# Kernel optimization log

Measured on AMD Instinct MI355X. Metric: run time of the kernel, lower is better.

The kernel has to match this reference:

```python
import jax, jax.numpy as jnp
import numpy as np

C = 256          # channels
NH = 8           # heads
DH = 64          # dim_head
NMEM = 4         # num_mem_kv
HIDDEN = NH * DH # 512
SCALE = DH ** (-0.5)


def _rmsnorm(x, gain):
    # F.normalize(x, dim=1) * gain * sqrt(C)  (scale-only RMS norm over channel dim)
    n = jnp.sqrt(jnp.sum(x * x, axis=1, keepdims=True))
    return x / jnp.maximum(n, 1e-12) * gain * (x.shape[1] ** 0.5)


def setup_inputs() -> dict:
    key = jax.random.key(0)
    ks = jax.random.split(key, 6)
    B, Hh, Ww = 16, 64, 64
    return {
        "x": jax.random.normal(ks[0], (B, C, Hh, Ww), jnp.float32),
        "gain1": jnp.ones((1, C, 1, 1), jnp.float32),
        "w_qkv": jax.random.normal(ks[1], (3 * HIDDEN, C), jnp.float32) * 0.02,
        "mem_kv": jax.random.normal(ks[2], (2, NH, DH, NMEM), jnp.float32),
        "w_out": jax.random.normal(ks[3], (C, HIDDEN), jnp.float32) * 0.02,
        "b_out": jnp.zeros((C,), jnp.float32),
        "gain2": jnp.ones((1, C, 1, 1), jnp.float32),
    }


def reference(x, gain1, w_qkv, mem_kv, w_out, b_out, gain2):
    B, _, Hh, Ww = x.shape
    N = Hh * Ww
    # pre-norm
    xn = _rmsnorm(x, gain1)
    # 1x1 conv QKV projection (no bias) == channel GEMM
    qkv = jnp.einsum('oc,bchw->bohw', w_qkv, xn)          # [B, 3*hidden, H, W]
    qkv = qkv.reshape(B, 3, NH, DH, N)                    # chunk + 'b (h c) x y -> b h c (x y)'
    q, k, v = qkv[:, 0], qkv[:, 1], qkv[:, 2]             # [B, h, d, N]
    # learned global memory kv, broadcast over batch
    mem_k = jnp.broadcast_to(mem_kv[0], (B, NH, DH, NMEM))
    mem_v = jnp.broadcast_to(mem_kv[1], (B, NH, DH, NMEM))
    k = jnp.concatenate([mem_k, k], axis=-1)              # [B, h, d, NMEM+N]
    v = jnp.concatenate([mem_v, v], axis=-1)
    # dual softmax: q over feature dim d, k over token dim n
    q = jax.nn.softmax(q, axis=-2) * SCALE
    k = jax.nn.softmax(k, axis=-1)
    # linear attention: O(N) context
    context = jnp.einsum('bhdn,bhen->bhde', k, v)         # [B, h, d, e]
    out = jnp.einsum('bhde,bhdn->bhen', context, q)       # [B, h, e, N]
    out = out.reshape(B, HIDDEN, Hh, Ww)
    # 1x1 conv out projection (with bias) + post RMSNorm
    out = jnp.einsum('oc,bchw->bohw', w_out, out) + b_out[None, :, None, None]
    return _rmsnorm(out, gain2)
```

## Files before the change

### kernel.cpp

```cpp
#include <hip/hip_runtime.h>

typedef __attribute__((ext_vector_type(8))) short bf16x8;
typedef __attribute__((ext_vector_type(4))) short bf16x4;
typedef __attribute__((ext_vector_type(4))) float f32x4;
typedef unsigned short u16;

constexpr int B_   = 16;
constexpr int C_   = 256;
constexpr int NH   = 8;
constexpr int DH   = 64;
constexpr int NMEM = 4;
constexpr int HID  = 512;
constexpr int QKVC = 1536;
constexpr int N_   = 4096;
constexpr int CTXS = 4224;

__device__ __forceinline__ u16 f2b(float f) {
  union { float f; unsigned u; } v{f};
  unsigned r = v.u + 0x7fff + ((v.u >> 16) & 1);
  return (u16)(r >> 16);
}
__device__ __forceinline__ float b2f(u16 h) {
  union { unsigned u; float f; } v; v.u = ((unsigned)h) << 16; return v.f;
}

__device__ __forceinline__ void gld_lds16(const u16* g, u16* l) {
  __builtin_amdgcn_global_load_lds(
      (const __attribute__((address_space(1))) unsigned*)g,
      (__attribute__((address_space(3))) unsigned*)l, 16, 0, 0);
}

__global__ void k_cvtw(const float* __restrict__ wq, const float* __restrict__ wo,
                       u16* __restrict__ wqb, u16* __restrict__ wob) {
  int i = blockIdx.x * 256 + threadIdx.x;
  for (int idx = i; idx < QKVC * C_; idx += gridDim.x * 256) wqb[idx] = f2b(wq[idx]);
  for (int idx = i; idx < C_ * HID; idx += gridDim.x * 256) wob[idx] = f2b(wo[idx]);
}

__global__ __launch_bounds__(256) void k_rms1(const float* __restrict__ x,
                                              const float* __restrict__ g1,
                                              u16* __restrict__ xbT) {
  int g = blockIdx.y;
  int n = blockIdx.x * 256 + threadIdx.x;
  const float* xp = x + (size_t)g * C_ * N_ + n;
  float ss = 0.f;
  #pragma unroll 8
  for (int c = 0; c < C_; ++c) { float v = xp[(size_t)c * N_]; ss += v * v; }
  float inv = 16.0f / fmaxf(sqrtf(ss), 1e-12f);
  u16* op = xbT + ((size_t)g * N_ + n) * C_;
  for (int c0 = 0; c0 < C_; c0 += 8) {
    union { bf16x8 v; u16 u[8]; } pk;
    #pragma unroll
    for (int j = 0; j < 8; ++j) pk.u[j] = f2b(xp[(size_t)(c0 + j) * N_] * inv * g1[c0 + j]);
    *(bf16x8*)(op + c0) = pk.v;
  }
}

__global__ __launch_bounds__(256) void k_kvctx(const u16* __restrict__ Wb,
                                               const u16* __restrict__ XT,
                                               float* __restrict__ ctxp) {
  constexpr int BK = 32;
  __shared__ __align__(16) u16 smem[16384];
  u16* Ws = smem;
  u16* Xs = smem + 4096;
  u16* Pl = smem;
  u16* Vl = smem + 8192;

  int cpx = gridDim.x >> 3;
  int bid = blockIdx.x;
  int L = (bid & 7) * cpx + (bid >> 3);
  int h = L & 7, nc = (L >> 3) & 7, g = L >> 6;
  int t = threadIdx.x, wave = t >> 6, lane = t & 63;
  int wm = wave >> 1, wn = wave & 1;
  int kg = lane >> 4, lr = lane & 15;

  const u16* WK = Wb + (size_t)(HID + h * DH) * C_;
  const u16* WV = Wb + (size_t)(2 * HID + h * DH) * C_;
  const u16* Xg = XT + ((size_t)g * N_ + nc * 512) * C_;

  int rloc = lane >> 2;
  int cswz = (lane & 3) ^ (rloc & 3);
  const u16* Wsrc = (wave < 2) ? WK : WV;
  int wrow0 = (wave * 32) & 63;

  f32x4 acc2[4];
  #pragma unroll
  for (int nf = 0; nf < 4; ++nf) acc2[nf] = (f32x4)0.f;
  float rs[4] = {0.f, 0.f, 0.f, 0.f};

  for (int it = 0; it < 4; ++it) {
    f32x4 acc[4][4];
    #pragma unroll
    for (int i = 0; i < 4; ++i)
      #pragma unroll
      for (int j = 0; j < 4; ++j) acc[i][j] = (f32x4)0.f;

    for (int k0 = 0; k0 < C_; k0 += BK) {
      #pragma unroll
      for (int q = 0; q < 2; ++q) {
        int rw = wrow0 + q * 16 + rloc;
        int rx = wave * 32 + q * 16 + rloc;
        gld_lds16(Wsrc + (size_t)rw * C_ + k0 + cswz * 8, Ws + (wave * 32 + q * 16) * 32);
        gld_lds16(Xg + (size_t)(it * 128 + rx) * C_ + k0 + cswz * 8, Xs + (wave * 32 + q * 16) * 32);
      }
      __syncthreads();
      bf16x8 a[4], bv[4];
      #pragma unroll
      for (int mf = 0; mf < 4; ++mf) {
        int r = wm * 64 + mf * 16 + lr;
        a[mf] = *(const bf16x8*)(Xs + r * 32 + ((kg ^ (r & 3)) * 8));
      }
      #pragma unroll
      for (int nf = 0; nf < 4; ++nf) {
        int r = wn * 64 + nf * 16 + lr;
        bv[nf] = *(const bf16x8*)(Ws + r * 32 + ((kg ^ (r & 3)) * 8));
      }
      #pragma unroll
      for (int mf = 0; mf < 4; ++mf)
        #pragma unroll
        for (int nf = 0; nf < 4; ++nf)
          acc[mf][nf] = __builtin_amdgcn_mfma_f32_16x16x32_bf16(a[mf], bv[nf], acc[mf][nf], 0, 0, 0);
      __syncthreads();
    }

    if (wn == 0) {
      #pragma unroll
      for (int mf = 0; mf < 4; ++mf) {
        int nb = wm * 64 + mf * 16 + kg * 4;
        int cc = nb >> 3, off = nb & 7;
        #pragma unroll
        for (int nf = 0; nf < 4; ++nf) {
          int d = nf * 16 + lr;
          float e0 = __expf(acc[mf][nf][0]);
          float e1 = __expf(acc[mf][nf][1]);
          float e2 = __expf(acc[mf][nf][2]);
          float e3 = __expf(acc[mf][nf][3]);
          rs[nf] += (e0 + e1) + (e2 + e3);
          union { bf16x4 v; u16 u[4]; } pk;
          pk.u[0] = f2b(e0); pk.u[1] = f2b(e1); pk.u[2] = f2b(e2); pk.u[3] = f2b(e3);
          *(bf16x4*)(Pl + d * 128 + ((cc ^ (d & 15)) * 8) + off) = pk.v;
        }
      }
    } else {
      #pragma unroll
      for (int mf = 0; mf < 4; ++mf) {
        int nb = wm * 64 + mf * 16 + kg * 4;
        int cc = nb >> 3, off = nb & 7;
        #pragma unroll
        for (int nf = 0; nf < 4; ++nf) {
          int e = nf * 16 + lr;
          union { bf16x4 v; u16 u[4]; } pk;
          pk.u[0] = f2b(acc[mf][nf][0]); pk.u[1] = f2b(acc[mf][nf][1]);
          pk.u[2] = f2b(acc[mf][nf][2]); pk.u[3] = f2b(acc[mf][nf][3]);
          *(bf16x4*)(Vl + e * 128 + ((cc ^ (e & 15)) * 8) + off) = pk.v;
        }
      }
    }
    __syncthreads();

    #pragma unroll
    for (int k = 0; k < 4; ++k) {
      int c = k * 4 + kg;
      bf16x8 af = *(const bf16x8*)(Pl + (wave * 16 + lr) * 128 + ((c ^ lr) * 8));
      #pragma unroll
      for (int nf = 0; nf < 4; ++nf) {
        bf16x8 bfv = *(const bf16x8*)(Vl + (nf * 16 + lr) * 128 + ((c ^ lr) * 8));
        acc2[nf] = __builtin_amdgcn_mfma_f32_16x16x32_bf16(af, bfv, acc2[nf], 0, 0, 0);
      }
    }
    __syncthreads();
  }

  float* cgp = ctxp + ((size_t)(g * NH + h) * 8 + nc) * CTXS;
  #pragma unroll
  for (int nf = 0; nf < 4; ++nf)
    #pragma unroll
    for (int j = 0; j < 4; ++j) {
      int d = wave * 16 + kg * 4 + j;
      int e = nf * 16 + lr;
      cgp[d * 64 + e] = acc2[nf][j];
    }
  if (wn == 0) {
    #pragma unroll
    for (int nf = 0; nf < 4; ++nf) {
      rs[nf] += __shfl_xor(rs[nf], 16);
      rs[nf] += __shfl_xor(rs[nf], 32);
    }
    if (lane < 16) {
      #pragma unroll
      for (int nf = 0; nf < 4; ++nf)
        cgp[4096 + wm * 64 + nf * 16 + lane] = rs[nf];
    }
  }
}

__global__ __launch_bounds__(256) void k_cfin(const float* __restrict__ ctxp,
                                              const float* __restrict__ memkv,
                                              u16* __restrict__ ctxTb) {
  int g = blockIdx.y, h = blockIdx.x;
  int t = threadIdx.x;
  __shared__ float emk[DH * NMEM];
  __shared__ float sd[DH];
  const float* mk = memkv + (size_t)h * DH * NMEM;
  const float* mv = memkv + (size_t)(NH + h) * DH * NMEM;
  const float* cp = ctxp + (size_t)(g * NH + h) * 8 * CTXS;
  emk[t] = __expf(mk[t]);
  __syncthreads();
  if (t < DH) {
    float s = 0.f;
    #pragma unroll
    for (int p = 0; p < 8; ++p)
      s += cp[p * CTXS + 4096 + t] + cp[p * CTXS + 4160 + t];
    #pragma unroll
    for (int j = 0; j < NMEM; ++j) s += emk[t * 4 + j];
    sd[t] = s;
  }
  __syncthreads();
  u16* ct = ctxTb + (size_t)(g * NH + h) * 4096;
  #pragma unroll
  for (int i = 0; i < 16; ++i) {
    int idx = t + 256 * i;
    int d = idx >> 6, e = idx & 63;
    float v = 0.f;
    #pragma unroll
    for (int p = 0; p < 8; ++p) v += cp[p * CTXS + idx];
    #pragma unroll
    for (int j = 0; j < NMEM; ++j) v += emk[d * 4 + j] * mv[e * 4 + j];
    ct[e * 64 + d] = f2b(v / sd[d]);
  }
}

__global__ __launch_bounds__(256) void k_qpv(const u16* __restrict__ Wq,
                                             const u16* __restrict__ XT,
                                             const u16* __restrict__ ctxTb,
                                             u16* __restrict__ attnT) {
  constexpr int BK = 32;
  __shared__ __align__(16) u16 smem[24576];
  u16* Ws = smem;
  u16* Xs = smem + 4096;
  u16* cl = smem + 16384;

  int cpx = gridDim.x >> 3;
  int bid = blockIdx.x;
  int L = (bid & 7) * cpx + (bid >> 3);
  int hh = L & 3, rest = L >> 2;
  int nc = rest & 31, g = rest >> 5;
  int t = threadIdx.x, wave = t >> 6, lane = t & 63;
  int wm = wave >> 1, wn = wave & 1;
  int kg = lane >> 4, lr = lane & 15;

  {
    const u16* cg = ctxTb + (size_t)(g * NH + hh * 2) * 4096;
    #pragma unroll
    for (int i = 0; i < 4; ++i) {
      int id = t + 256 * i;
      int r = id >> 3, c = id & 7;
      *(bf16x8*)(cl + (r >> 6) * 4096 + (r & 63) * 64 + ((c ^ (r & 7)) * 8)) =
          *(const bf16x8*)(cg + id * 8);
    }
  }

  const u16* Ag = Wq + (size_t)(hh * 128) * C_;
  const u16* Bg = XT + ((size_t)g * N_ + nc * 128) * C_;
  int rloc = lane >> 2;
  int cswz = (lane & 3) ^ (rloc & 3);

  f32x4 acc[4][4];
  #pragma unroll
  for (int i = 0; i < 4; ++i)
    #pragma unroll
    for (int j = 0; j < 4; ++j) acc[i][j] = (f32x4)0.f;

  for (int k0 = 0; k0 < C_; k0 += BK) {
    #pragma unroll
    for (int q = 0; q < 2; ++q) {
      int r = wave * 32 + q * 16 + rloc;
      gld_lds16(Ag + (size_t)r * C_ + k0 + cswz * 8, Ws + (wave * 32 + q * 16) * 32);
      gld_lds16(Bg + (size_t)r * C_ + k0 + cswz * 8, Xs + (wave * 32 + q * 16) * 32);
    }
    __syncthreads();
    bf16x8 a[4], bv[4];
    #pragma unroll
    for (int mf = 0; mf < 4; ++mf) {
      int r = wm * 64 + mf * 16 + lr;
      a[mf] = *(const bf16x8*)(Ws + r * 32 + ((kg ^ (r & 3)) * 8));
    }
    #pragma unroll
    for (int nf = 0; nf < 4; ++nf) {
      int r = wn * 64 + nf * 16 + lr;
      bv[nf] = *(const bf16x8*)(Xs + r * 32 + ((kg ^ (r & 3)) * 8));
    }
    #pragma unroll
    for (int mf = 0; mf < 4; ++mf)
      #pragma unroll
      for (int nf = 0; nf < 4; ++nf)
        acc[mf][nf] = __builtin_amdgcn_mfma_f32_16x16x32_bf16(a[mf], bv[nf], acc[mf][nf], 0, 0, 0);
    __syncthreads();
  }

  float colsum[4];
  #pragma unroll
  for (int nf = 0; nf < 4; ++nf) {
    float s = 0.f;
    #pragma unroll
    for (int mf = 0; mf < 4; ++mf)
      #pragma unroll
      for (int j = 0; j < 4; ++j) {
        float e = __expf(acc[mf][nf][j]);
        acc[mf][nf][j] = e;
        s += e;
      }
    colsum[nf] = s;
  }
  #pragma unroll
  for (int nf = 0; nf < 4; ++nf) {
    colsum[nf] += __shfl_xor(colsum[nf], 16);
    colsum[nf] += __shfl_xor(colsum[nf], 32);
  }
  u16* qh = smem + wm * 8192;
  #pragma unroll
  for (int nf = 0; nf < 4; ++nf) {
    float invs = 0.125f / colsum[nf];
    int n = wn * 64 + nf * 16 + lr;
    #pragma unroll
    for (int mf = 0; mf < 4; ++mf)
      #pragma unroll
      for (int jp = 0; jp < 2; ++jp) {
        int d0 = mf * 16 + kg * 4 + jp * 2;
        u16 lo = f2b(acc[mf][nf][jp * 2] * invs);
        u16 hi = f2b(acc[mf][nf][jp * 2 + 1] * invs);
        unsigned pk = (unsigned)lo | ((unsigned)hi << 16);
        int idx = n * 64 + (((d0 >> 3) ^ (n & 7)) * 8) + (d0 & 7);
        *(unsigned*)(qh + idx) = pk;
      }
  }
  __syncthreads();

  int hcl = wave >> 1, nh2 = wave & 1;
  const u16* qh2 = smem + hcl * 8192;
  const u16* clh = cl + hcl * 4096;
  f32x4 acc2[4][4];
  #pragma unroll
  for (int i = 0; i < 4; ++i)
    #pragma unroll
    for (int j = 0; j < 4; ++j) acc2[i][j] = (f32x4)0.f;

  #pragma unroll
  for (int kk = 0; kk < 2; ++kk) {
    int c = kk * 4 + kg;
    bf16x8 a2[4], b2[4];
    #pragma unroll
    for (int mf = 0; mf < 4; ++mf) {
      int rn = nh2 * 64 + mf * 16 + lr;
      a2[mf] = *(const bf16x8*)(qh2 + rn * 64 + ((c ^ (rn & 7)) * 8));
    }
    #pragma unroll
    for (int nf = 0; nf < 4; ++nf) {
      int re = nf * 16 + lr;
      b2[nf] = *(const bf16x8*)(clh + re * 64 + ((c ^ (re & 7)) * 8));
    }
    #pragma unroll
    for (int mf = 0; mf < 4; ++mf)
      #pragma unroll
      for (int nf = 0; nf < 4; ++nf)
        acc2[mf][nf] = __builtin_amdgcn_mfma_f32_16x16x32_bf16(a2[mf], b2[nf], acc2[mf][nf], 0, 0, 0);
  }

  int h = hh * 2 + hcl;
  u16* op = attnT + ((size_t)g * N_ + nc * 128) * HID + h * 64;
  #pragma unroll
  for (int mf = 0; mf < 4; ++mf)
    #pragma unroll
    for (int nf = 0; nf < 4; ++nf)
      #pragma unroll
      for (int j = 0; j < 4; ++j) {
        int n = nh2 * 64 + mf * 16 + kg * 4 + j;
        int e = nf * 16 + lr;
        op[(size_t)n * HID + e] = f2b(acc2[mf][nf][j]);
      }
}

__global__ __launch_bounds__(256) void k_out(const u16* __restrict__ Wb,
                                             const u16* __restrict__ AT,
                                             const float* __restrict__ bias,
                                             const float* __restrict__ g2,
                                             float* __restrict__ out) {
  constexpr int BN = 128, BK = 32;
  __shared__ __align__(16) u16 As[256 * BK];
  __shared__ __align__(16) u16 Bs[BN * BK];
  __shared__ float part[4][BN];
  int g  = blockIdx.y;
  int n0 = blockIdx.x * BN;
  int t = threadIdx.x, wave = t >> 6, lane = t & 63;
  int kg = lane >> 4, lr = lane & 15;

  const u16* Bg = AT + ((size_t)g * N_ + n0) * HID;

  int rloc = lane >> 2;
  int cswz = (lane & 3) ^ (rloc & 3);

  f32x4 acc[4][8];
  #pragma unroll
  for (int i = 0; i < 4; ++i)
    #pragma unroll
    for (int j = 0; j < 8; ++j) acc[i][j] = (f32x4)0.f;

  for (int k0 = 0; k0 < HID; k0 += BK) {
    #pragma unroll
    for (int q = 0; q < 4; ++q) {
      int r = wave * 64 + q * 16 + rloc;
      gld_lds16(Wb + (size_t)r * HID + k0 + cswz * 8, As + (wave * 64 + q * 16) * 32);
    }
    #pragma unroll
    for (int q = 0; q < 2; ++q) {
      int r = wave * 32 + q * 16 + rloc;
      gld_lds16(Bg + (size_t)r * HID + k0 + cswz * 8, Bs + (wave * 32 + q * 16) * 32);
    }
    __syncthreads();
    bf16x8 a[4], bv[8];
    #pragma unroll
    for (int mf = 0; mf < 4; ++mf) {
      int r = wave * 64 + mf * 16 + lr;
      a[mf] = *(const bf16x8*)(As + r * 32 + ((kg ^ (r & 3)) * 8));
    }
    #pragma unroll
    for (int nf = 0; nf < 8; ++nf) {
      int r = nf * 16 + lr;
      bv[nf] = *(const bf16x8*)(Bs + r * 32 + ((kg ^ (r & 3)) * 8));
    }
    #pragma unroll
    for (int mf = 0; mf < 4; ++mf)
      #pragma unroll
      for (int nf = 0; nf < 8; ++nf)
        acc[mf][nf] = __builtin_amdgcn_mfma_f32_16x16x32_bf16(a[mf], bv[nf], acc[mf][nf], 0, 0, 0);
    __syncthreads();
  }
  float colsq[8] = {0.f, 0.f, 0.f, 0.f, 0.f, 0.f, 0.f, 0.f};
  #pragma unroll
  for (int mf = 0; mf < 4; ++mf)
    #pragma unroll
    for (int j = 0; j < 4; ++j) {
      int row = wave * 64 + mf * 16 + kg * 4 + j;
      float bs = bias[row];
      #pragma unroll
      for (int nf = 0; nf < 8; ++nf) {
        float v = acc[mf][nf][j] + bs;
        acc[mf][nf][j] = v;
        colsq[nf] += v * v;
      }
    }
  #pragma unroll
  for (int nf = 0; nf < 8; ++nf) {
    colsq[nf] += __shfl_xor(colsq[nf], 16);
    colsq[nf] += __shfl_xor(colsq[nf], 32);
  }
  if (kg == 0) {
    #pragma unroll
    for (int nf = 0; nf < 8; ++nf) part[wave][nf * 16 + lr] = colsq[nf];
  }
  __syncthreads();
  float* og = out + (size_t)g * C_ * N_ + n0;
  #pragma unroll
  for (int nf = 0; nf < 8; ++nf) {
    int col = nf * 16 + lr;
    float tot = part[0][col] + part[1][col] + part[2][col] + part[3][col];
    float invn = 16.0f / fmaxf(sqrtf(tot), 1e-12f);
    #pragma unroll
    for (int mf = 0; mf < 4; ++mf)
      #pragma unroll
      for (int j = 0; j < 4; ++j) {
        int row = wave * 64 + mf * 16 + kg * 4 + j;
        og[(size_t)row * N_ + col] = acc[mf][nf][j] * invn * g2[row];
      }
  }
}

extern "C" void kernel_launch(void* const* d_in, const int* in_sizes, int n_in,
                              void* d_out, int out_size, void* d_ws, size_t ws_size,
                              hipStream_t stream) {
  (void)in_sizes; (void)n_in; (void)out_size;
  const float* x      = (const float*)d_in[0];
  const float* gain1  = (const float*)d_in[1];
  const float* w_qkv  = (const float*)d_in[2];
  const float* mem_kv = (const float*)d_in[3];
  const float* w_out  = (const float*)d_in[4];
  const float* b_out  = (const float*)d_in[5];
  const float* gain2  = (const float*)d_in[6];
  float* out = (float*)d_out;

  char* ws = (char*)d_ws;
  u16* wqkvb = (u16*)ws;
  u16* woutb = (u16*)(ws + 786432);
  size_t shared_b = 1048576;

  const size_t xbT_b   = (size_t)N_ * C_ * 2;
  const size_t attnT_b = (size_t)HID * N_ * 2;
  const size_t ctxp_b  = (size_t)NH * 8 * CTXS * 4;
  const size_t ctxT_b  = (size_t)NH * 4096 * 2;
  const size_t per_b   = xbT_b + attnT_b + ctxp_b + ctxT_b;

  int G = 16;
  while (G > 1 && shared_b + (size_t)G * per_b > ws_size) G >>= 1;

  char* base = ws + shared_b;
  u16*   xbT   = (u16*)base;
  u16*   attnT = (u16*)(base + (size_t)G * xbT_b);
  float* ctxp  = (float*)(base + (size_t)G * (xbT_b + attnT_b));
  u16*   ctxTb = (u16*)(base + (size_t)G * (xbT_b + attnT_b + ctxp_b));

  k_cvtw<<<256, 256, 0, stream>>>(w_qkv, w_out, wqkvb, woutb);

  for (int b0 = 0; b0 < B_; b0 += G) {
    const float* xc = x + (size_t)b0 * C_ * N_;
    float*       oc = out + (size_t)b0 * C_ * N_;
    k_rms1  <<<dim3(N_ / 256, G),  256, 0, stream>>>(xc, gain1, xbT);
    k_kvctx <<<dim3(64 * G),       256, 0, stream>>>(wqkvb, xbT, ctxp);
    k_cfin  <<<dim3(NH, G),        256, 0, stream>>>(ctxp, mem_kv, ctxTb);
    k_qpv   <<<dim3(4 * 32 * G),   256, 0, stream>>>(wqkvb, xbT, ctxTb, attnT);
    k_out   <<<dim3(N_ / 128, G),  256, 0, stream>>>(woutb, attnT, b_out, gain2, oc);
  }
}
```

Before: 199.4 us.

## Double GEMM K-tile to 64 with 8-way swizzle and vectorize RMS norm loads

The three MFMA GEMM kernels (kvctx, qpv, out) now stage a 64-wide K tile per iteration instead of 32, using an 8-chunk XOR swizzle. This halves the number of barrier pairs per K loop and does two MFMA k-steps per staged tile, at the cost of more LDS per block. Separately, the pre-norm kernel has each thread handle 4 adjacent pixels with float4 loads and launches a quarter as many blocks. That widens global reads but leaves fewer threads in flight for a bandwidth-bound pass.

New measurement: 205.0 us. 2.8% more time.

```diff
diff --git a/kernel.cpp b/kernel.cpp
--- a/kernel.cpp
+++ b/kernel.cpp
@@ -41,28 +41,41 @@
                                               const float* __restrict__ g1,
                                               u16* __restrict__ xbT) {
   int g = blockIdx.y;
-  int n = blockIdx.x * 256 + threadIdx.x;
-  const float* xp = x + (size_t)g * C_ * N_ + n;
-  float ss = 0.f;
-  #pragma unroll 8
-  for (int c = 0; c < C_; ++c) { float v = xp[(size_t)c * N_]; ss += v * v; }
-  float inv = 16.0f / fmaxf(sqrtf(ss), 1e-12f);
-  u16* op = xbT + ((size_t)g * N_ + n) * C_;
+  int n0 = (blockIdx.x * 256 + threadIdx.x) * 4;
+  const float* xg = x + (size_t)g * C_ * N_;
+  float ss0 = 0.f, ss1 = 0.f, ss2 = 0.f, ss3 = 0.f;
+  #pragma unroll 4
+  for (int c = 0; c < C_; ++c) {
+    float4 v = *(const float4*)(xg + (size_t)c * N_ + n0);
+    ss0 += v.x * v.x; ss1 += v.y * v.y; ss2 += v.z * v.z; ss3 += v.w * v.w;
+  }
+  float inv0 = 16.0f / fmaxf(sqrtf(ss0), 1e-12f);
+  float inv1 = 16.0f / fmaxf(sqrtf(ss1), 1e-12f);
+  float inv2 = 16.0f / fmaxf(sqrtf(ss2), 1e-12f);
+  float inv3 = 16.0f / fmaxf(sqrtf(ss3), 1e-12f);
+  u16* op = xbT + ((size_t)g * N_ + n0) * C_;
   for (int c0 = 0; c0 < C_; c0 += 8) {
-    union { bf16x8 v; u16 u[8]; } pk;
-    #pragma unroll
-    for (int j = 0; j < 8; ++j) pk.u[j] = f2b(xp[(size_t)(c0 + j) * N_] * inv * g1[c0 + j]);
-    *(bf16x8*)(op + c0) = pk.v;
+    union { bf16x8 v; u16 u[8]; } p0, p1, p2, p3;
+    #pragma unroll
+    for (int j = 0; j < 8; ++j) {
+      float4 v = *(const float4*)(xg + (size_t)(c0 + j) * N_ + n0);
+      float gc = g1[c0 + j];
+      p0.u[j] = f2b(v.x * inv0 * gc); p1.u[j] = f2b(v.y * inv1 * gc);
+      p2.u[j] = f2b(v.z * inv2 * gc); p3.u[j] = f2b(v.w * inv3 * gc);
+    }
+    *(bf16x8*)(op + c0)          = p0.v;
+    *(bf16x8*)(op + C_ + c0)     = p1.v;
+    *(bf16x8*)(op + 2 * C_ + c0) = p2.v;
+    *(bf16x8*)(op + 3 * C_ + c0) = p3.v;
   }
 }
 
 __global__ __launch_bounds__(256) void k_kvctx(const u16* __restrict__ Wb,
                                                const u16* __restrict__ XT,
                                                float* __restrict__ ctxp) {
-  constexpr int BK = 32;
   __shared__ __align__(16) u16 smem[16384];
   u16* Ws = smem;
-  u16* Xs = smem + 4096;
+  u16* Xs = smem + 8192;
   u16* Pl = smem;
   u16* Vl = smem + 8192;
 
@@ -78,10 +91,9 @@
   const u16* WV = Wb + (size_t)(2 * HID + h * DH) * C_;
   const u16* Xg = XT + ((size_t)g * N_ + nc * 512) * C_;
 
-  int rloc = lane >> 2;
-  int cswz = (lane & 3) ^ (rloc & 3);
+  int rl8 = lane >> 3;
+  int cs8 = (lane & 7) ^ rl8;
   const u16* Wsrc = (wave < 2) ? WK : WV;
-  int wrow0 = (wave * 32) & 63;
 
   f32x4 acc2[4];
   #pragma unroll
@@ -95,31 +107,36 @@
       #pragma unroll
       for (int j = 0; j < 4; ++j) acc[i][j] = (f32x4)0.f;
 
-    for (int k0 = 0; k0 < C_; k0 += BK) {
-      #pragma unroll
-      for (int q = 0; q < 2; ++q) {
-        int rw = wrow0 + q * 16 + rloc;
-        int rx = wave * 32 + q * 16 + rloc;
-        gld_lds16(Wsrc + (size_t)rw * C_ + k0 + cswz * 8, Ws + (wave * 32 + q * 16) * 32);
-        gld_lds16(Xg + (size_t)(it * 128 + rx) * C_ + k0 + cswz * 8, Xs + (wave * 32 + q * 16) * 32);
+    for (int k0 = 0; k0 < C_; k0 += 64) {
+      #pragma unroll
+      for (int q = 0; q < 4; ++q) {
+        int rb = wave * 32 + q * 8;
+        int rw = (rb & 63) + rl8;
+        int rx = it * 128 + rb + rl8;
+        gld_lds16(Wsrc + (size_t)rw * C_ + k0 + cs8 * 8, Ws + rb * 64);
+        gld_lds16(Xg + (size_t)rx * C_ + k0 + cs8 * 8, Xs + rb * 64);
       }
       __syncthreads();
-      bf16x8 a[4], bv[4];
-      #pragma unroll
-      for (int mf = 0; mf < 4; ++mf) {
-        int r = wm * 64 + mf * 16 + lr;
-        a[mf] = *(const bf16x8*)(Xs + r * 32 + ((kg ^ (r & 3)) * 8));
-      }
-      #pragma unroll
-      for (int nf = 0; nf < 4; ++nf) {
-        int r = wn * 64 + nf * 16 + lr;
-        bv[nf] = *(const bf16x8*)(Ws + r * 32 + ((kg ^ (r & 3)) * 8));
-      }
-      #pragma unroll
-      for (int mf = 0; mf < 4; ++mf)
-        #pragma unroll
-        for (int nf = 0; nf < 4; ++nf)
-          acc[mf][nf] = __builtin_amdgcn_mfma_f32_16x16x32_bf16(a[mf], bv[nf], acc[mf][nf], 0, 0, 0);
+      #pragma unroll
+      for (int ks = 0; ks < 2; ++ks) {
+        int ch = ks * 4 + kg;
+        bf16x8 a[4], bv[4];
+        #pragma unroll
+        for (int mf = 0; mf < 4; ++mf) {
+          int r = wm * 64 + mf * 16 + lr;
+          a[mf] = *(const bf16x8*)(Xs + r * 64 + ((ch ^ (r & 7)) * 8));
+        }
+        #pragma unroll
+        for (int nf = 0; nf < 4; ++nf) {
+          int r = wn * 64 + nf * 16 + lr;
+          bv[nf] = *(const bf16x8*)(Ws + r * 64 + ((ch ^ (r & 7)) * 8));
+        }
+        #pragma unroll
+        for (int mf = 0; mf < 4; ++mf)
+          #pragma unroll
+          for (int nf = 0; nf < 4; ++nf)
+            acc[mf][nf] = __builtin_amdgcn_mfma_f32_16x16x32_bf16(a[mf], bv[nf], acc[mf][nf], 0, 0, 0);
+      }
       __syncthreads();
     }
 
@@ -234,10 +251,9 @@
                                              const u16* __restrict__ XT,
                                              const u16* __restrict__ ctxTb,
                                              u16* __restrict__ attnT) {
-  constexpr int BK = 32;
   __shared__ __align__(16) u16 smem[24576];
   u16* Ws = smem;
-  u16* Xs = smem + 4096;
+  u16* Xs = smem + 8192;
   u16* cl = smem + 16384;
 
   int cpx = gridDim.x >> 3;
@@ -262,8 +278,8 @@
 
   const u16* Ag = Wq + (size_t)(hh * 128) * C_;
   const u16* Bg = XT + ((size_t)g * N_ + nc * 128) * C_;
-  int rloc = lane >> 2;
-  int cswz = (lane & 3) ^ (rloc & 3);
+  int rl8 = lane >> 3;
+  int cs8 = (lane & 7) ^ rl8;
 
   f32x4 acc[4][4];
   #pragma unroll
@@ -271,30 +287,34 @@
     #pragma unroll
     for (int j = 0; j < 4; ++j) acc[i][j] = (f32x4)0.f;
 
-  for (int k0 = 0; k0 < C_; k0 += BK) {
-    #pragma unroll
-    for (int q = 0; q < 2; ++q) {
-      int r = wave * 32 + q * 16 + rloc;
-      gld_lds16(Ag + (size_t)r * C_ + k0 + cswz * 8, Ws + (wave * 32 + q * 16) * 32);
-      gld_lds16(Bg + (size_t)r * C_ + k0 + cswz * 8, Xs + (wave * 32 + q * 16) * 32);
+  for (int k0 = 0; k0 < C_; k0 += 64) {
+    #pragma unroll
+    for (int q = 0; q < 4; ++q) {
+      int rb = wave * 32 + q * 8;
+      gld_lds16(Ag + (size_t)(rb + rl8) * C_ + k0 + cs8 * 8, Ws + rb * 64);
+      gld_lds16(Bg + (size_t)(rb + rl8) * C_ + k0 + cs8 * 8, Xs + rb * 64);
     }
     __syncthreads();
-    bf16x8 a[4], bv[4];
-    #pragma unroll
-    for (int mf = 0; mf < 4; ++mf) {
-      int r = wm * 64 + mf * 16 + lr;
-      a[mf] = *(const bf16x8*)(Ws + r * 32 + ((kg ^ (r & 3)) * 8));
-    }
-    #pragma unroll
-    for (int nf = 0; nf < 4; ++nf) {
-      int r = wn * 64 + nf * 16 + lr;
-      bv[nf] = *(const bf16x8*)(Xs + r * 32 + ((kg ^ (r & 3)) * 8));
-    }
-    #pragma unroll
-    for (int mf = 0; mf < 4; ++mf)
-      #pragma unroll
-      for (int nf = 0; nf < 4; ++nf)
-        acc[mf][nf] = __builtin_amdgcn_mfma_f32_16x16x32_bf16(a[mf], bv[nf], acc[mf][nf], 0, 0, 0);
+    #pragma unroll
+    for (int ks = 0; ks < 2; ++ks) {
+      int ch = ks * 4 + kg;
+      bf16x8 a[4], bv[4];
+      #pragma unroll
+      for (int mf = 0; mf < 4; ++mf) {
+        int r = wm * 64 + mf * 16 + lr;
+        a[mf] = *(const bf16x8*)(Ws + r * 64 + ((ch ^ (r & 7)) * 8));
+      }
+      #pragma unroll
+      for (int nf = 0; nf < 4; ++nf) {
+        int r = wn * 64 + nf * 16 + lr;
+        bv[nf] = *(const bf16x8*)(Xs + r * 64 + ((ch ^ (r & 7)) * 8));
+      }
+      #pragma unroll
+      for (int mf = 0; mf < 4; ++mf)
+        #pragma unroll
+        for (int nf = 0; nf < 4; ++nf)
+          acc[mf][nf] = __builtin_amdgcn_mfma_f32_16x16x32_bf16(a[mf], bv[nf], acc[mf][nf], 0, 0, 0);
+    }
     __syncthreads();
   }
 
@@ -385,9 +405,9 @@
                                              const float* __restrict__ bias,
                                              const float* __restrict__ g2,
                                              float* __restrict__ out) {
-  constexpr int BN = 128, BK = 32;
-  __shared__ __align__(16) u16 As[256 * BK];
-  __shared__ __align__(16) u16 Bs[BN * BK];
+  constexpr int BN = 128;
+  __shared__ __align__(16) u16 As[256 * 64];
+  __shared__ __align__(16) u16 Bs[BN * 64];
   __shared__ float part[4][BN];
   int g  = blockIdx.y;
   int n0 = blockIdx.x * BN;
@@ -396,8 +416,8 @@
 
   const u16* Bg = AT + ((size_t)g * N_ + n0) * HID;
 
-  int rloc = lane >> 2;
-  int cswz = (lane & 3) ^ (rloc & 3);
+  int rl8 = lane >> 3;
+  int cs8 = (lane & 7) ^ rl8;
 
   f32x4 acc[4][8];
   #pragma unroll
@@ -405,34 +425,38 @@
     #pragma unroll
     for (int j = 0; j < 8; ++j) acc[i][j] = (f32x4)0.f;
 
-  for (int k0 = 0; k0 < HID; k0 += BK) {
+  for (int k0 = 0; k0 < HID; k0 += 64) {
+    #pragma unroll
+    for (int q = 0; q < 8; ++q) {
+      int rb = wave * 64 + q * 8;
+      gld_lds16(Wb + (size_t)(rb + rl8) * HID + k0 + cs8 * 8, As + rb * 64);
+    }
     #pragma unroll
     for (int q = 0; q < 4; ++q) {
-      int r = wave * 64 + q * 16 + rloc;
-      gld_lds16(Wb + (size_t)r * HID + k0 + cswz * 8, As + (wave * 64 + q * 16) * 32);
-    }
-    #pragma unroll
-    for (int q = 0; q < 2; ++q) {
-      int r = wave * 32 + q * 16 + rloc;
-      gld_lds16(Bg + (size_t)r * HID + k0 + cswz * 8, Bs + (wave * 32 + q * 16) * 32);
+      int rb = wave * 32 + q * 8;
+      gld_lds16(Bg + (size_t)(rb + rl8) * HID + k0 + cs8 * 8, Bs + rb * 64);
     }
     __syncthreads();
-    bf16x8 a[4], bv[8];
-    #pragma unroll
-    for (int mf = 0; mf < 4; ++mf) {
-      int r = wave * 64 + mf * 16 + lr;
-      a[mf] = *(const bf16x8*)(As + r * 32 + ((kg ^ (r & 3)) * 8));
-    }
-    #pragma unroll
-    for (int nf = 0; nf < 8; ++nf) {
-      int r = nf * 16 + lr;
-      bv[nf] = *(const bf16x8*)(Bs + r * 32 + ((kg ^ (r & 3)) * 8));
-    }
-    #pragma unroll
-    for (int mf = 0; mf < 4; ++mf)
-      #pragma unroll
-      for (int nf = 0; nf < 8; ++nf)
-        acc[mf][nf] = __builtin_amdgcn_mfma_f32_16x16x32_bf16(a[mf], bv[nf], acc[mf][nf], 0, 0, 0);
+    #pragma unroll
+    for (int ks = 0; ks < 2; ++ks) {
+      int ch = ks * 4 + kg;
+      bf16x8 a[4], bv[8];
+      #pragma unroll
+      for (int mf = 0; mf < 4; ++mf) {
+        int r = wave * 64 + mf * 16 + lr;
+        a[mf] = *(const bf16x8*)(As + r * 64 + ((ch ^ (r & 7)) * 8));
+      }
+      #pragma unroll
+      for (int nf = 0; nf < 8; ++nf) {
+        int r = nf * 16 + lr;
+        bv[nf] = *(const bf16x8*)(Bs + r * 64 + ((ch ^ (r & 7)) * 8));
+      }
+      #pragma unroll
+      for (int mf = 0; mf < 4; ++mf)
+        #pragma unroll
+        for (int nf = 0; nf < 8; ++nf)
+          acc[mf][nf] = __builtin_amdgcn_mfma_f32_16x16x32_bf16(a[mf], bv[nf], acc[mf][nf], 0, 0, 0);
+    }
     __syncthreads();
   }
   float colsq[8] = {0.f, 0.f, 0.f, 0.f, 0.f, 0.f, 0.f, 0.f};
@@ -513,7 +537,7 @@
   for (int b0 = 0; b0 < B_; b0 += G) {
     const float* xc = x + (size_t)b0 * C_ * N_;
     float*       oc = out + (size_t)b0 * C_ * N_;
-    k_rms1  <<<dim3(N_ / 256, G),  256, 0, stream>>>(xc, gain1, xbT);
+    k_rms1  <<<dim3(N_ / 1024, G), 256, 0, stream>>>(xc, gain1, xbT);
     k_kvctx <<<dim3(64 * G),       256, 0, stream>>>(wqkvb, xbT, ctxp);
     k_cfin  <<<dim3(NH, G),        256, 0, stream>>>(ctxp, mem_kv, ctxTb);
     k_qpv   <<<dim3(4 * 32 * G),   256, 0, stream>>>(wqkvb, xbT, ctxTb, attnT);
```
